# Kernel optimization log

Hardware: AMD Instinct MI355X
Metric: run time of the kernel (lower is better)

Reference implementation:

```python
import jax, jax.numpy as jnp
import numpy as np

HEADS = 8
DIM_HEAD = 64
NUM_MEM_KV = 4

def rmsnorm(x, g):
    # F.normalize(x, dim=1) * g * sqrt(C): L2-normalize over channel dim with eps clamp
    n = jnp.sqrt(jnp.sum(x * x, axis=1, keepdims=True))
    return x / jnp.maximum(n, 1e-12) * g * (x.shape[1] ** 0.5)

def setup_inputs() -> dict:
    key = jax.random.key(0)
    ks = jax.random.split(key, 7)
    b, c, h, w = 32, 512, 32, 32
    hidden = HEADS * DIM_HEAD
    x = jax.random.normal(ks[0], (b, c, h, w), jnp.float32)
    g_in = 1.0 + 0.02 * jax.random.normal(ks[1], (1, c, 1, 1), jnp.float32)
    w_qkv = jax.random.normal(ks[2], (3 * hidden, c), jnp.float32) * (c ** -0.5)
    mem_kv = jax.random.normal(ks[3], (2, HEADS, DIM_HEAD, NUM_MEM_KV), jnp.float32)
    w_out = jax.random.normal(ks[4], (c, hidden), jnp.float32) * (hidden ** -0.5)
    b_out = 0.01 * jax.random.normal(ks[5], (c,), jnp.float32)
    g_out = 1.0 + 0.02 * jax.random.normal(ks[6], (1, c, 1, 1), jnp.float32)
    return {"x": x, "g_in": g_in, "w_qkv": w_qkv, "mem_kv": mem_kv,
            "w_out": w_out, "b_out": b_out, "g_out": g_out}

def reference(x, g_in, w_qkv, mem_kv, w_out, b_out, g_out):
    b, c, h, w = x.shape
    scale = DIM_HEAD ** -0.5
    xn = rmsnorm(x, g_in)
    # 1x1 conv (no bias) == channel GEMM
    qkv = jnp.einsum('bchw,oc->bohw', xn, w_qkv)
    q, k, v = jnp.split(qkv, 3, axis=1)
    to_heads = lambda t: t.reshape(b, HEADS, DIM_HEAD, h * w)  # b (h c) x y -> b h c (xy)
    q, k, v = map(to_heads, (q, k, v))
    mk = jnp.broadcast_to(mem_kv[0], (b,) + mem_kv[0].shape)
    mv = jnp.broadcast_to(mem_kv[1], (b,) + mem_kv[1].shape)
    k = jnp.concatenate([mk, k], axis=-1)
    v = jnp.concatenate([mv, v], axis=-1)
    q = jax.nn.softmax(q, axis=-2) * scale   # softmax over feature dim d
    k = jax.nn.softmax(k, axis=-1)           # softmax over sequence dim n
    context = jnp.einsum('bhdn,bhen->bhde', k, v)
    out = jnp.einsum('bhde,bhdn->bhen', context, q)
    out = out.reshape(b, HEADS * DIM_HEAD, h, w)
    out = jnp.einsum('bchw,oc->bohw', out, w_out) + b_out[None, :, None, None]
    return rmsnorm(out, g_out)
```

## Files before the change

kernel.cpp:

```cpp
#include <hip/hip_runtime.h>
#include <hip/hip_bf16.h>


#define AS1 __attribute__((address_space(1)))
#define AS3 __attribute__((address_space(3)))

using short8 = __attribute__((ext_vector_type(8))) short;
using usht4  = __attribute__((ext_vector_type(4))) unsigned short;
using f32x4  = __attribute__((ext_vector_type(4))) float;

__device__ __forceinline__ unsigned short f2bf(float f) {
  unsigned int u = __float_as_uint(f);
  u += 0x7fffu + ((u >> 16) & 1u);
  return (unsigned short)(u >> 16);
}
__device__ __forceinline__ float bf2f(unsigned short s) {
  return __uint_as_float(((unsigned int)s) << 16);
}

__global__ __launch_bounds__(256, 4)
void norm_r(const float* __restrict__ X, float* __restrict__ R) {
  __shared__ float part[8][32];
  const int t = threadIdx.x;
  const int b = blockIdx.x >> 5;
  const int pos0 = (blockIdx.x & 31) * 32;
  const int p = t & 31, cg = t >> 5;
  const float* xp = X + ((size_t)b * 512 + (size_t)cg * 64) * 1024 + pos0 + p;
  float s = 0.f;
#pragma unroll 8
  for (int i = 0; i < 64; ++i) {
    float v = xp[(size_t)i * 1024];
    s += v * v;
  }
  part[cg][p] = s;
  __syncthreads();
  if (t < 32) {
    float tot = 0.f;
#pragma unroll
    for (int j = 0; j < 8; ++j) tot += part[j][t];
    R[(size_t)b * 1024 + pos0 + t] = 22.627416998f / fmaxf(sqrtf(tot), 1e-12f);
  }
}

__global__ __launch_bounds__(256, 4)
void norm_r_bf16(const unsigned short* __restrict__ X, float* __restrict__ R) {
  __shared__ float part[16][64];
  const int t = threadIdx.x;
  const int b = blockIdx.x >> 4;
  const int pos0 = (blockIdx.x & 15) * 64;
  const int pg = t & 15, cg = t >> 4;
  const unsigned short* xp =
      X + ((size_t)b * 512 + (size_t)cg * 32) * 1024 + pos0 + pg * 4;
  float s0 = 0.f, s1 = 0.f, s2 = 0.f, s3 = 0.f;
#pragma unroll 8
  for (int i = 0; i < 32; ++i) {
    usht4 v = *(const usht4*)(xp + (size_t)i * 1024);
    float a = bf2f(v.x), bb = bf2f(v.y), c = bf2f(v.z), d = bf2f(v.w);
    s0 += a * a; s1 += bb * bb; s2 += c * c; s3 += d * d;
  }
  part[cg][pg * 4 + 0] = s0;
  part[cg][pg * 4 + 1] = s1;
  part[cg][pg * 4 + 2] = s2;
  part[cg][pg * 4 + 3] = s3;
  __syncthreads();
  if (t < 64) {
    float tot = 0.f;
#pragma unroll
    for (int j = 0; j < 16; ++j) tot += part[j][t];
    R[(size_t)b * 1024 + pos0 + t] = 22.627416998f / fmaxf(sqrtf(tot), 1e-12f);
  }
}

__global__ __launch_bounds__(256, 4)
void xn_transpose(const float* __restrict__ X, const float* __restrict__ R,
                  unsigned short* __restrict__ XT) {
  __shared__ float tile[64][65];
  const int t = threadIdx.x;
  const int b = blockIdx.z, cb = blockIdx.y, pb = blockIdx.x;
  {
    const int p = t & 63, cg = t >> 6;
    const float r = R[(size_t)b * 1024 + pb * 64 + p];
    const float* xp = X + ((size_t)b * 512 + (size_t)(cb * 64 + cg * 16)) * 1024 + pb * 64 + p;
#pragma unroll
    for (int i = 0; i < 16; ++i)
      tile[cg * 16 + i][p] = xp[(size_t)i * 1024] * r;
  }
  __syncthreads();
  {
    const int c = t & 63, pg = t >> 6;
    unsigned short* op = XT + ((size_t)b * 1024 + pb * 64 + pg * 16) * 512 + cb * 64 + c;
#pragma unroll
    for (int i = 0; i < 16; ++i)
      op[(size_t)i * 512] = f2bf(tile[c][pg * 16 + i]);
  }
}

__global__ __launch_bounds__(256, 4)
void cast_wqkv(const float* __restrict__ W, const float* __restrict__ g,
               unsigned short* __restrict__ O) {
  int i = blockIdx.x * 256 + threadIdx.x;
  O[i] = f2bf(W[i] * g[i & 511]);
}
__global__ __launch_bounds__(256, 4)
void cast_w(const float* __restrict__ W, unsigned short* __restrict__ O, int n) {
  int i = blockIdx.x * 256 + threadIdx.x;
  if (i < n) O[i] = f2bf(W[i]);
}

template <int MTOT, bool SPLIT3, bool BIAS>
__global__ __launch_bounds__(256, 2)
void gemm_bt(const unsigned short* __restrict__ A,
             const unsigned short* __restrict__ Ball,
             unsigned short* __restrict__ O0, unsigned short* __restrict__ O1,
             unsigned short* __restrict__ O2, const float* __restrict__ bias) {
  __shared__ char smem[34816];
  unsigned short* lA = (unsigned short*)smem;
  unsigned short* lB = lA + 128 * 64;
  const int t = threadIdx.x;
  const int lane = t & 63, w = t >> 6;
  const int wm = w >> 1, wn = w & 1;
  const int mt = blockIdx.x >> 3, nt = blockIdx.x & 7;
  const int b = blockIdx.y;
  const unsigned short* Ag = A + (size_t)(mt * 128) * 512;
  const unsigned short* Bg = Ball + ((size_t)b * 1024 + (size_t)nt * 128) * 512;
  const int scol = (lane & 7) * 8;
  f32x4 acc[4][4] = {};

  for (int kt = 0; kt < 8; ++kt) {
    const unsigned short* As = Ag + kt * 64 + scol;
    const unsigned short* Bs = Bg + kt * 64 + scol;
#pragma unroll
    for (int i = 0; i < 4; ++i) {
      const int r = w * 32 + i * 8 + (lane >> 3);
      __builtin_amdgcn_global_load_lds(
          (const AS1 unsigned int*)(As + (size_t)r * 512),
          (AS3 unsigned int*)(lA + (w * 32 + i * 8) * 64), 16, 0, 0);
      __builtin_amdgcn_global_load_lds(
          (const AS1 unsigned int*)(Bs + (size_t)r * 512),
          (AS3 unsigned int*)(lB + (w * 32 + i * 8) * 64), 16, 0, 0);
    }
    __syncthreads();
#pragma unroll
    for (int ks = 0; ks < 2; ++ks) {
      short8 af[4], bfv[4];
#pragma unroll
      for (int i = 0; i < 4; ++i)
        af[i] = *(const short8*)(lA + (wm * 64 + i * 16 + (lane & 15)) * 64 +
                                 ks * 32 + (lane >> 4) * 8);
#pragma unroll
      for (int j = 0; j < 4; ++j)
        bfv[j] = *(const short8*)(lB + (wn * 64 + j * 16 + (lane & 15)) * 64 +
                                  ks * 32 + (lane >> 4) * 8);
#pragma unroll
      for (int i = 0; i < 4; ++i)
#pragma unroll
        for (int j = 0; j < 4; ++j)
          acc[i][j] = __builtin_amdgcn_mfma_f32_16x16x32_bf16(af[i], bfv[j],
                                                              acc[i][j], 0, 0, 0);
    }
    __syncthreads();
  }

  unsigned short* Cst = (unsigned short*)smem;
#pragma unroll
  for (int i = 0; i < 4; ++i)
#pragma unroll
    for (int j = 0; j < 4; ++j)
#pragma unroll
      for (int r = 0; r < 4; ++r) {
        const int row = wm * 64 + i * 16 + (lane >> 4) * 4 + r;
        const int col = wn * 64 + j * 16 + (lane & 15);
        float v = acc[i][j][r];
        if (BIAS) v += bias[mt * 128 + row];
        Cst[row * 136 + col] = f2bf(v);
      }
  __syncthreads();
  unsigned short* Og;
  if (SPLIT3) {
    const int sec = mt >> 2;
    unsigned short* base = (sec == 0) ? O0 : ((sec == 1) ? O1 : O2);
    Og = base + ((size_t)b * 512 + (size_t)(mt & 3) * 128) * 1024 + (size_t)nt * 128;
  } else {
    Og = O0 + ((size_t)b * MTOT + (size_t)mt * 128) * 1024 + (size_t)nt * 128;
  }
#pragma unroll
  for (int k = 0; k < 8; ++k) {
    const int f = t + k * 256;
    const int row = f >> 4, c8 = f & 15;
    short8 v = *(const short8*)(Cst + row * 136 + c8 * 8);
    *(short8*)(Og + (size_t)row * 1024 + c8 * 8) = v;
  }
}

__global__ __launch_bounds__(256, 2)
void attn_kernel(const unsigned short* __restrict__ Qp,
                 const unsigned short* __restrict__ Kp,
                 const unsigned short* __restrict__ Vp,
                 const float* __restrict__ memkv,
                 unsigned short* __restrict__ outT) {
  __shared__ char smem[36608];
  unsigned short* bufA = (unsigned short*)smem;
  unsigned short* bufB = (unsigned short*)(smem + 9216);
  float* Pl   = (float*)(smem + 18432);
  float* Pc   = (float*)(smem + 18432);
  float* csS  = (float*)(smem + 19456);
  float* msum = (float*)(smem + 35072);
  float* rsI  = (float*)(smem + 36096);
  const int t = threadIdx.x;
  const int lane = t & 63, wave = t >> 6;
  const int b = blockIdx.x >> 3, h = blockIdx.x & 7;
  const size_t hb = ((size_t)b * 512 + (size_t)h * 64) * 1024;
  const unsigned short* Qg = Qp + hb;
  const unsigned short* Kg = Kp + hb;
  const unsigned short* Vg = Vp + hb;
  const float* mk = memkv + (size_t)h * 256;
  const float* mv = memkv + 2048 + (size_t)h * 256;

  float rpart[16];
#pragma unroll
  for (int i = 0; i < 16; ++i) rpart[i] = 0.f;
  f32x4 cacc[4] = {};

  for (int it = 0; it < 17; ++it) {
    if (it == 0) {
      const int d = t & 63, j = t >> 6;
      const float ev = __expf(mk[d * 4 + j]);
      msum[d * 4 + j] = ev;
      bufA[d * 72 + j] = f2bf(ev);
      bufB[d * 72 + j] = f2bf(mv[d * 4 + j]);
      for (int c2 = 4 + j; c2 < 64; c2 += 4) {
        bufA[d * 72 + c2] = 0;
        bufB[d * 72 + c2] = 0;
      }
    } else {
      const int c0 = (it - 1) * 64;
#pragma unroll
      for (int i = 0; i < 16; ++i) {
        const int d = wave * 16 + i;
        const float ev = __expf(bf2f(Kg[(size_t)d * 1024 + c0 + lane]));
        rpart[i] += ev;
        bufA[d * 72 + lane] = f2bf(ev);
        bufB[d * 72 + lane] = Vg[(size_t)d * 1024 + c0 + lane];
      }
    }
    __syncthreads();
#pragma unroll
    for (int ks = 0; ks < 2; ++ks) {
      short8 a = *(const short8*)(bufA + (wave * 16 + (lane & 15)) * 72 +
                                  ks * 32 + (lane >> 4) * 8);
#pragma unroll
      for (int et = 0; et < 4; ++et) {
        short8 bb = *(const short8*)(bufB + (et * 16 + (lane & 15)) * 72 +
                                     ks * 32 + (lane >> 4) * 8);
        cacc[et] = __builtin_amdgcn_mfma_f32_16x16x32_bf16(a, bb, cacc[et], 0, 0, 0);
      }
    }
    __syncthreads();
  }

#pragma unroll
  for (int i = 0; i < 16; ++i) Pl[(wave * 16 + i) * 65 + lane] = rpart[i];
  __syncthreads();
  if (t < 64) {
    float s = 0.f;
#pragma unroll 8
    for (int j = 0; j < 64; ++j) s += Pl[t * 65 + j];
    s += msum[t * 4] + msum[t * 4 + 1] + msum[t * 4 + 2] + msum[t * 4 + 3];
    rsI[t] = 1.0f / s;
  }
  __syncthreads();

  unsigned short* CT = bufB;
#pragma unroll
  for (int et = 0; et < 4; ++et)
#pragma unroll
    for (int r = 0; r < 4; ++r) {
      const int d = wave * 16 + (lane >> 4) * 4 + r;
      const int e = et * 16 + (lane & 15);
      CT[e * 72 + d] = f2bf(cacc[et][r] * rsI[d]);
    }
  __syncthreads();

  short8 a0 = *(const short8*)(CT + (wave * 16 + (lane & 15)) * 72 + (lane >> 4) * 8);
  short8 a1 = *(const short8*)(CT + (wave * 16 + (lane & 15)) * 72 + 32 + (lane >> 4) * 8);
  unsigned short* oBase = outT + (size_t)b * 1024 * 512 + h * 64;

  for (int pt = 0; pt < 16; ++pt) {
    {
      const int p = lane, dq = wave;
      float cp = 0.f;
#pragma unroll
      for (int i2 = 0; i2 < 8; ++i2) {
        const int d0 = dq * 16 + i2 * 2;
        const float e0 = __expf(bf2f(Qg[(size_t)d0 * 1024 + pt * 64 + p]));
        const float e1 = __expf(bf2f(Qg[(size_t)(d0 + 1) * 1024 + pt * 64 + p]));
        cp += e0 + e1;
        const unsigned int pk =
            (unsigned int)f2bf(e0) | ((unsigned int)f2bf(e1) << 16);
        *(unsigned int*)(bufA + p * 72 + d0) = pk;
      }
      Pc[dq * 64 + p] = cp;
    }
    __syncthreads();
    if (t < 64) csS[t] = 0.125f / (Pc[t] + Pc[64 + t] + Pc[128 + t] + Pc[192 + t]);
    __syncthreads();
#pragma unroll
    for (int ps = 0; ps < 4; ++ps) {
      f32x4 oc = {};
      short8 b0 = *(const short8*)(bufA + (ps * 16 + (lane & 15)) * 72 + (lane >> 4) * 8);
      short8 b1 = *(const short8*)(bufA + (ps * 16 + (lane & 15)) * 72 + 32 + (lane >> 4) * 8);
      oc = __builtin_amdgcn_mfma_f32_16x16x32_bf16(a0, b0, oc, 0, 0, 0);
      oc = __builtin_amdgcn_mfma_f32_16x16x32_bf16(a1, b1, oc, 0, 0, 0);
      const float cs = csS[ps * 16 + (lane & 15)];
      const unsigned long long pk =
          (unsigned long long)f2bf(oc[0] * cs) |
          ((unsigned long long)f2bf(oc[1] * cs) << 16) |
          ((unsigned long long)f2bf(oc[2] * cs) << 32) |
          ((unsigned long long)f2bf(oc[3] * cs) << 48);
      const int p = pt * 64 + ps * 16 + (lane & 15);
      *(unsigned long long*)(oBase + (size_t)p * 512 + wave * 16 + (lane >> 4) * 4) = pk;
    }
    __syncthreads();
  }
}

__global__ __launch_bounds__(256, 4)
void final_scale_bf16(const unsigned short* __restrict__ P,
                      const float* __restrict__ R, const float* __restrict__ G,
                      float* __restrict__ O) {
  const size_t f = ((size_t)blockIdx.x * 256 + threadIdx.x) * 4;
  const int p = (int)(f & 1023);
  const int c = (int)((f >> 10) & 511);
  const int b = (int)(f >> 19);
  usht4 v = *(const usht4*)(P + f);
  const f32x4 r = *(const f32x4*)(R + (size_t)b * 1024 + p);
  const float g = G[c];
  f32x4 o;
  o.x = bf2f(v.x) * r.x * g;
  o.y = bf2f(v.y) * r.y * g;
  o.z = bf2f(v.z) * r.z * g;
  o.w = bf2f(v.w) * r.w * g;
  *(f32x4*)(O + f) = o;
}

extern "C" void kernel_launch(void* const* d_in, const int* in_sizes, int n_in,
                              void* d_out, int out_size, void* d_ws, size_t ws_size,
                              hipStream_t stream) {
  (void)in_sizes; (void)n_in; (void)out_size; (void)ws_size;
  const float* x     = (const float*)d_in[0];
  const float* g_in  = (const float*)d_in[1];
  const float* w_qkv = (const float*)d_in[2];
  const float* memkv = (const float*)d_in[3];
  const float* w_out = (const float*)d_in[4];
  const float* b_out = (const float*)d_in[5];
  const float* g_out = (const float*)d_in[6];
  float* out = (float*)d_out;

  char* ws = (char*)d_ws;
  float* r1           = (float*)ws;
  float* r2           = (float*)(ws + 131072);
  unsigned short* wqb = (unsigned short*)(ws + 262144);
  unsigned short* wob = (unsigned short*)(ws + 1835008);
  unsigned short* xnT = (unsigned short*)(ws + 2359296);
  unsigned short* Qp  = (unsigned short*)(ws + 35913728);
  unsigned short* outT = xnT;
  unsigned short* pre  = Qp;
  unsigned short* Kp  = (unsigned short*)d_out;
  unsigned short* Vp  = (unsigned short*)d_out + 16777216;

  norm_r<<<1024, 256, 0, stream>>>(x, r1);
  xn_transpose<<<dim3(16, 8, 32), 256, 0, stream>>>(x, r1, xnT);
  cast_wqkv<<<3072, 256, 0, stream>>>(w_qkv, g_in, wqb);
  cast_w<<<1024, 256, 0, stream>>>(w_out, wob, 262144);
  gemm_bt<1536, true, false><<<dim3(96, 32), 256, 0, stream>>>(
      wqb, xnT, Qp, Kp, Vp, nullptr);
  attn_kernel<<<256, 256, 0, stream>>>(Qp, Kp, Vp, memkv, outT);
  gemm_bt<512, false, true><<<dim3(32, 32), 256, 0, stream>>>(
      wob, outT, pre, nullptr, nullptr, b_out);
  norm_r_bf16<<<512, 256, 0, stream>>>(pre, r2);
  final_scale_bf16<<<16384, 256, 0, stream>>>(pre, r2, g_out, out);
}
```

Measured before the change: 290.6 us.

## Vectorize loads/stores in norm, transpose, attention; XOR-swizzle GEMM LDS

The norm kernel now reads four floats per load with more channel groups. The transpose writes eight bf16 values per store instead of scalar 2-byte stores. The GEMM applies an XOR swizzle to the LDS column layout to reduce bank conflicts on fragment reads. The attention kernel loads K and V as 16-byte vectors and keeps only two partial row sums per thread, which shrinks the final reduction. The aim is fewer memory transactions and fewer LDS conflicts, at the cost of more complex indexing. The transpose now reads the tile column-wise, which may cause LDS bank conflicts.

```diff
diff --git a/kernel.cpp b/kernel.cpp
--- a/kernel.cpp
+++ b/kernel.cpp
@@ -20,24 +20,27 @@
 
 __global__ __launch_bounds__(256, 4)
 void norm_r(const float* __restrict__ X, float* __restrict__ R) {
-  __shared__ float part[8][32];
+  __shared__ float part[32][33];
   const int t = threadIdx.x;
   const int b = blockIdx.x >> 5;
   const int pos0 = (blockIdx.x & 31) * 32;
-  const int p = t & 31, cg = t >> 5;
-  const float* xp = X + ((size_t)b * 512 + (size_t)cg * 64) * 1024 + pos0 + p;
-  float s = 0.f;
-#pragma unroll 8
-  for (int i = 0; i < 64; ++i) {
-    float v = xp[(size_t)i * 1024];
+  const int pg = t & 7, cg = t >> 3;
+  const float* xp = X + ((size_t)b * 512 + (size_t)cg * 16) * 1024 + pos0 + pg * 4;
+  f32x4 s = {0.f, 0.f, 0.f, 0.f};
+#pragma unroll
+  for (int i = 0; i < 16; ++i) {
+    f32x4 v = *(const f32x4*)(xp + (size_t)i * 1024);
     s += v * v;
   }
-  part[cg][p] = s;
+  part[cg][pg * 4 + 0] = s.x;
+  part[cg][pg * 4 + 1] = s.y;
+  part[cg][pg * 4 + 2] = s.z;
+  part[cg][pg * 4 + 3] = s.w;
   __syncthreads();
   if (t < 32) {
     float tot = 0.f;
 #pragma unroll
-    for (int j = 0; j < 8; ++j) tot += part[j][t];
+    for (int j = 0; j < 32; ++j) tot += part[j][t];
     R[(size_t)b * 1024 + pos0 + t] = 22.627416998f / fmaxf(sqrtf(tot), 1e-12f);
   }
 }
@@ -86,12 +89,14 @@
       tile[cg * 16 + i][p] = xp[(size_t)i * 1024] * r;
   }
   __syncthreads();
-  {
-    const int c = t & 63, pg = t >> 6;
-    unsigned short* op = XT + ((size_t)b * 1024 + pb * 64 + pg * 16) * 512 + cb * 64 + c;
-#pragma unroll
-    for (int i = 0; i < 16; ++i)
-      op[(size_t)i * 512] = f2bf(tile[c][pg * 16 + i]);
+#pragma unroll
+  for (int k = 0; k < 2; ++k) {
+    const int idx = k * 256 + t;
+    const int p = idx >> 3, c8 = idx & 7;
+    short8 v;
+#pragma unroll
+    for (int j = 0; j < 8; ++j) v[j] = (short)f2bf(tile[c8 * 8 + j][p]);
+    *(short8*)(XT + ((size_t)b * 1024 + pb * 64 + p) * 512 + cb * 64 + c8 * 8) = v;
   }
 }
 
@@ -123,7 +128,7 @@
   const int b = blockIdx.y;
   const unsigned short* Ag = A + (size_t)(mt * 128) * 512;
   const unsigned short* Bg = Ball + ((size_t)b * 1024 + (size_t)nt * 128) * 512;
-  const int scol = (lane & 7) * 8;
+  const int scol = ((lane & 7) ^ (lane >> 3)) * 8;
   f32x4 acc[4][4] = {};
 
   for (int kt = 0; kt < 8; ++kt) {
@@ -142,15 +147,14 @@
     __syncthreads();
 #pragma unroll
     for (int ks = 0; ks < 2; ++ks) {
+      const int pch = ((ks * 4 + (lane >> 4)) ^ (lane & 7)) * 8;
       short8 af[4], bfv[4];
 #pragma unroll
       for (int i = 0; i < 4; ++i)
-        af[i] = *(const short8*)(lA + (wm * 64 + i * 16 + (lane & 15)) * 64 +
-                                 ks * 32 + (lane >> 4) * 8);
+        af[i] = *(const short8*)(lA + (wm * 64 + i * 16 + (lane & 15)) * 64 + pch);
 #pragma unroll
       for (int j = 0; j < 4; ++j)
-        bfv[j] = *(const short8*)(lB + (wn * 64 + j * 16 + (lane & 15)) * 64 +
-                                  ks * 32 + (lane >> 4) * 8);
+        bfv[j] = *(const short8*)(lB + (wn * 64 + j * 16 + (lane & 15)) * 64 + pch);
 #pragma unroll
       for (int i = 0; i < 4; ++i)
 #pragma unroll
@@ -203,7 +207,7 @@
   unsigned short* bufB = (unsigned short*)(smem + 9216);
   float* Pl   = (float*)(smem + 18432);
   float* Pc   = (float*)(smem + 18432);
-  float* csS  = (float*)(smem + 19456);
+  float* csS  = (float*)(smem + 21504);
   float* msum = (float*)(smem + 35072);
   float* rsI  = (float*)(smem + 36096);
   const int t = threadIdx.x;
@@ -216,9 +220,7 @@
   const float* mk = memkv + (size_t)h * 256;
   const float* mv = memkv + 2048 + (size_t)h * 256;
 
-  float rpart[16];
-#pragma unroll
-  for (int i = 0; i < 16; ++i) rpart[i] = 0.f;
+  float rsum[2] = {0.f, 0.f};
   f32x4 cacc[4] = {};
 
   for (int it = 0; it < 17; ++it) {
@@ -235,12 +237,21 @@
     } else {
       const int c0 = (it - 1) * 64;
 #pragma unroll
-      for (int i = 0; i < 16; ++i) {
-        const int d = wave * 16 + i;
-        const float ev = __expf(bf2f(Kg[(size_t)d * 1024 + c0 + lane]));
-        rpart[i] += ev;
-        bufA[d * 72 + lane] = f2bf(ev);
-        bufB[d * 72 + lane] = Vg[(size_t)d * 1024 + c0 + lane];
+      for (int z = 0; z < 2; ++z) {
+        const int d = z * 32 + (t >> 3), ch = t & 7;
+        short8 kv = *(const short8*)(Kg + (size_t)d * 1024 + c0 + ch * 8);
+        short8 pk;
+        float ssum = 0.f;
+#pragma unroll
+        for (int j = 0; j < 8; ++j) {
+          const float e = __expf(bf2f((unsigned short)kv[j]));
+          ssum += e;
+          pk[j] = (short)f2bf(e);
+        }
+        rsum[z] += ssum;
+        *(short8*)(bufA + d * 72 + ch * 8) = pk;
+        short8 vv = *(const short8*)(Vg + (size_t)d * 1024 + c0 + ch * 8);
+        *(short8*)(bufB + d * 72 + ch * 8) = vv;
       }
     }
     __syncthreads();
@@ -258,13 +269,13 @@
     __syncthreads();
   }
 
-#pragma unroll
-  for (int i = 0; i < 16; ++i) Pl[(wave * 16 + i) * 65 + lane] = rpart[i];
+  Pl[t]       = rsum[0];
+  Pl[256 + t] = rsum[1];
   __syncthreads();
   if (t < 64) {
     float s = 0.f;
-#pragma unroll 8
-    for (int j = 0; j < 64; ++j) s += Pl[t * 65 + j];
+#pragma unroll
+    for (int ch = 0; ch < 8; ++ch) s += Pl[t * 8 + ch];
     s += msum[t * 4] + msum[t * 4 + 1] + msum[t * 4 + 2] + msum[t * 4 + 3];
     rsI[t] = 1.0f / s;
   }
```

Measured after the change: 277.9 us. -4.4%, faster.
